# Kernel tuning notes

Hardware: AMD Instinct MI355X
Metric: run time of the kernel (lower is better)

The kernel has to match this reference:

```python
import jax, jax.numpy as jnp
import numpy as np

NUM_HEADS = 8
EPS = 1e-12  # torch F.normalize eps


def _l2norm(t):
    n = jnp.linalg.norm(t, axis=-1, keepdims=True)
    return t / jnp.maximum(n, EPS)


def setup_inputs() -> dict:
    key = jax.random.key(0)
    k1, k2, k3 = jax.random.split(key, 3)
    B, T, N, D = 16, 12, 1024, 128
    x = jax.random.normal(k1, (B, T, N, D), dtype=jnp.float32)
    # Linear(model_dim, 3*model_dim, bias=False): stored as (D, 3D) for x @ W
    W_qkv = jax.random.normal(k2, (D, 3 * D), dtype=jnp.float32) * (1.0 / np.sqrt(D))
    W_out = jax.random.normal(k3, (D, D), dtype=jnp.float32) * (1.0 / np.sqrt(D))
    b_out = jnp.zeros((D,), dtype=jnp.float32)
    return {"x": x, "W_qkv": W_qkv, "W_out": W_out, "b_out": b_out}


def reference(x, W_qkv, W_out, b_out):
    B, T, N, D = x.shape
    H = NUM_HEADS
    hd = D // H
    qkv = x @ W_qkv                                  # (B,T,N,3D)
    q, k, v = jnp.split(qkv, 3, axis=-1)
    # split heads + flatten (B,T) -> b = B*T, matching torch stack/flatten
    qs = _l2norm(q.reshape(B * T, N, H, hd))          # (b,N,H,m)
    ks = _l2norm(k.reshape(B * T, N, H, hd))
    vs = v.reshape(B * T, N, H, hd)
    # linear attention: running kv sum + normalizer
    kvs = jnp.einsum('blhm,blhd->bhmd', ks, vs)       # (b,H,m,d)
    attn_num = jnp.einsum('bnhm,bhmd->bnhd', qs, kvs) + N * vs
    ks_sum = jnp.sum(ks, axis=1)                      # (b,H,m)
    normalizer = jnp.einsum('bnhm,bhm->bnh', qs, ks_sum)[..., None] + N
    out = attn_num / normalizer                       # (b,N,H,d)
    out = out.reshape(B, T, N, D)
    return out @ W_out + b_out
```

## Files before the change

kernel.cpp:

```cpp
#include <hip/hip_runtime.h>
#include <hip/hip_bf16.h>

#define NBATCH 192
#define SEQ    1024
#define DIM    128
#define NH     8
#define EPS    1e-12f

typedef short bf16x8 __attribute__((ext_vector_type(8)));
typedef float f32x4  __attribute__((ext_vector_type(4)));

#define KVS_F   393216
#define ZERO_F  417792
#define WSWT_OFF ((size_t)ZERO_F * 4)
#define XB_OFF   (WSWT_OFF + 131072)
#define XB_SHPB  32768
#define WS_NEED  (XB_OFF + (size_t)768 * XB_SHPB * 2)

static __device__ __forceinline__ unsigned short f2bf(float f) {
    unsigned u = __builtin_bit_cast(unsigned, f);
    u += 0x7fff + ((u >> 16) & 1);
    return (unsigned short)(u >> 16);
}

static __device__ __forceinline__ unsigned pk2(float a, float b) {
    __hip_bfloat162 h = __float22bfloat162_rn(make_float2(a, b));
    unsigned r;
    __builtin_memcpy(&r, &h, 4);
    return r;
}
static __device__ __forceinline__ unsigned short bf1(float a) {
    __hip_bfloat16 h = __float2bfloat16(a);
    unsigned short r;
    __builtin_memcpy(&r, &h, 2);
    return r;
}

template <int CTRL>
static __device__ __forceinline__ float dpp_add(float v) {
    int j = __builtin_amdgcn_mov_dpp(__builtin_bit_cast(int, v), CTRL, 0xf, 0xf, false);
    return v + __builtin_bit_cast(float, j);
}
static __device__ __forceinline__ float r16sum(float v) {
    v = dpp_add<0xB1>(v);
    v = dpp_add<0x4E>(v);
    v = dpp_add<0x141>(v);
    v = dpp_add<0x140>(v);
    return v;
}

static __device__ __forceinline__ int strip_addr(int row, int el) {
    return row * 32 + ((((el >> 3) ^ (row & 3)) << 3) | (el & 7));
}

static __device__ __forceinline__ uint2 pack4(float a, float b, float c, float d) {
    uint2 r;
    r.x = pk2(a, b);
    r.y = pk2(c, d);
    return r;
}

static __device__ __forceinline__ bf16x8 cvt8(float4 a, float4 b) {
    uint4 u;
    u.x = pk2(a.x, a.y); u.y = pk2(a.z, a.w);
    u.z = pk2(b.x, b.y); u.w = pk2(b.z, b.w);
    return __builtin_bit_cast(bf16x8, u);
}

static __device__ __forceinline__ bf16x8 gfrag(const unsigned short* __restrict__ wT,
                                               int ct, int ks, int lane) {
    return *reinterpret_cast<const bf16x8*>(wT + ((ct * 4 + ks) * 64 + lane) * 8);
}

__global__ __launch_bounds__(256) void k0_prep(const float* __restrict__ Wqkv,
                                               const float* __restrict__ Wout,
                                               float* __restrict__ zero_p,
                                               unsigned short* __restrict__ wsWT) {
    int bid = blockIdx.x, t = threadIdx.x;
    if (bid < 1632) { zero_p[bid * 256 + t] = 0.0f; return; }
    int i = (bid - 1632) * 256 + t;
    int which = i >> 14, e = i & 16383;
    int j = e & 7, f = e >> 3;
    int n15 = f & 15, q = (f >> 4) & 3, ks = (f >> 6) & 3, ct = f >> 8;
    int k = ks * 32 + q * 8 + j, n = ct * 16 + n15;
    float v = (which < 3) ? Wqkv[k * 384 + which * 128 + n] : Wout[k * 128 + n];
    wsWT[i] = f2bf(v);
}

__global__ __launch_bounds__(512, 4) void k1_kv(const float* __restrict__ x,
                                                const unsigned short* __restrict__ wsWT,
                                                float* __restrict__ kvs_ws,
                                                float* __restrict__ kssum_ws,
                                                unsigned short* __restrict__ xb,
                                                int writeXb) {
    __shared__ float redf[16384];
    __shared__ unsigned short strips[8192];
    int t = threadIdx.x, w = t >> 6, lane = t & 63, q = lane >> 4, n15 = lane & 15;
    int b = blockIdx.x >> 2, seg = blockIdx.x & 3;
    const unsigned short* wkT = wsWT + 16384;
    const unsigned short* wvT = wsWT + 32768;
    unsigned short* knS = strips + w * 1024;
    unsigned short* vS  = knS + 512;

    bf16x8 ah[2][4];
#pragma unroll
    for (int rs = 0; rs < 2; ++rs) {
        int row = seg * 256 + w * 32 + rs * 16 + n15;
        const float* xr = x + (size_t)(b * SEQ + row) * DIM;
#pragma unroll
        for (int ks = 0; ks < 4; ++ks) {
            float4 p0 = *reinterpret_cast<const float4*>(xr + ks * 32 + q * 8);
            float4 p1 = *reinterpret_cast<const float4*>(xr + ks * 32 + q * 8 + 4);
            ah[rs][ks] = cvt8(p0, p1);
        }
    }
    if (writeXb) {
        unsigned short* xo = xb + (size_t)blockIdx.x * XB_SHPB + t * 8;
#pragma unroll
        for (int rs = 0; rs < 2; ++rs)
#pragma unroll
            for (int ks = 0; ks < 4; ++ks)
                *reinterpret_cast<uint4*>(xo + (rs * 4 + ks) * 4096) =
                    __builtin_bit_cast(uint4, ah[rs][ks]);
    }

#pragma unroll 1
    for (int ct = 0; ct < 8; ++ct) {
        f32x4 ka[2] = {(f32x4){0,0,0,0}, (f32x4){0,0,0,0}};
        f32x4 va[2] = {(f32x4){0,0,0,0}, (f32x4){0,0,0,0}};
#pragma unroll
        for (int ks = 0; ks < 4; ++ks) {
            bf16x8 kb = gfrag(wkT, ct, ks, lane);
            bf16x8 vb = gfrag(wvT, ct, ks, lane);
#pragma unroll
            for (int rs = 0; rs < 2; ++rs) {
                ka[rs] = __builtin_amdgcn_mfma_f32_16x16x32_bf16(ah[rs][ks], kb, ka[rs], 0, 0, 0);
                va[rs] = __builtin_amdgcn_mfma_f32_16x16x32_bf16(ah[rs][ks], vb, va[rs], 0, 0, 0);
            }
        }
        float ksum = 0.f;
#pragma unroll
        for (int rs = 0; rs < 2; ++rs) {
            float kn[4];
#pragma unroll
            for (int r = 0; r < 4; ++r) {
                float val = ka[rs][r];
                float ssq = r16sum(val * val);
                float di  = 1.0f / fmaxf(sqrtf(ssq), EPS);
                kn[r] = val * di;
                ksum += kn[r];
            }
            *reinterpret_cast<uint2*>(knS + strip_addr(n15, rs * 16 + q * 4)) =
                pack4(kn[0], kn[1], kn[2], kn[3]);
            *reinterpret_cast<uint2*>(vS + strip_addr(n15, rs * 16 + q * 4)) =
                pack4(va[rs][0], va[rs][1], va[rs][2], va[rs][3]);
        }
        bf16x8 aK = *reinterpret_cast<const bf16x8*>(knS + strip_addr(n15, q * 8));
        bf16x8 bV = *reinterpret_cast<const bf16x8*>(vS + strip_addr(n15, q * 8));
        f32x4 kacc = __builtin_amdgcn_mfma_f32_16x16x32_bf16(aK, bV, (f32x4){0,0,0,0}, 0, 0, 0);
#pragma unroll
        for (int r = 0; r < 4; ++r)
            redf[w * 2048 + ct * 256 + (q * 4 + r) * 16 + n15] = kacc[r];
        float s = ksum;
        s += __shfl_xor(s, 16); s += __shfl_xor(s, 32);
        if (lane < 16) atomicAdd(&kssum_ws[b * 128 + ct * 16 + n15], s);
    }

    __syncthreads();
#pragma unroll
    for (int i = 0; i < 4; ++i) {
        int el = i * 512 + t;
        float s = 0.f;
#pragma unroll
        for (int ww = 0; ww < 8; ++ww) s += redf[ww * 2048 + el];
        atomicAdd(&kvs_ws[b * 2048 + el], s);
    }
}

template <int XB>
__global__ __launch_bounds__(512, 4) void k2_out(const float* __restrict__ x,
                                                 const unsigned short* __restrict__ wsWT,
                                                 const float* __restrict__ kvs_ws,
                                                 const float* __restrict__ kssum_ws,
                                                 const float* __restrict__ bout,
                                                 float* __restrict__ out,
                                                 const unsigned short* __restrict__ xb) {
    __shared__ unsigned short lds[24576];
    unsigned short* kvsT   = lds;
    unsigned short* strips = lds + 4096;
    unsigned short* tile   = lds + 8192;
    int t = threadIdx.x, w = t >> 6, lane = t & 63, q = lane >> 4, n15 = lane & 15;
    int b = blockIdx.x >> 2, seg = blockIdx.x & 3, rowbase = seg * 256;
    const unsigned short* wqT = wsWT;
    const unsigned short* wvT = wsWT + 32768;
    const unsigned short* woT = wsWT + 49152;

    {
        int row = t >> 2, part = t & 3, h = row >> 4, d = row & 15;
        unsigned es[8];
#pragma unroll
        for (int j = 0; j < 8; j += 2) {
            int m0 = part * 8 + j;
            float lo = (m0     < 16) ? kvs_ws[b * 2048 + h * 256 + m0 * 16 + d]       : 0.f;
            float hi = (m0 + 1 < 16) ? kvs_ws[b * 2048 + h * 256 + (m0 + 1) * 16 + d] : 0.f;
            es[j] = pk2(lo, hi);
        }
        uint4 v = {es[0], es[2], es[4], es[6]};
        *reinterpret_cast<uint4*>(kvsT + row * 32 + ((part ^ (row & 3)) << 3)) = v;
    }

    bf16x8 ah[2][4];
    if (XB) {
        const unsigned short* xi = xb + (size_t)blockIdx.x * XB_SHPB + t * 8;
#pragma unroll
        for (int rs = 0; rs < 2; ++rs)
#pragma unroll
            for (int ks = 0; ks < 4; ++ks)
                ah[rs][ks] = *reinterpret_cast<const bf16x8*>(xi + (rs * 4 + ks) * 4096);
    } else {
#pragma unroll
        for (int rs = 0; rs < 2; ++rs) {
            int row = rowbase + w * 32 + rs * 16 + n15;
            const float* xr = x + (size_t)(b * SEQ + row) * DIM;
#pragma unroll
            for (int ks = 0; ks < 4; ++ks) {
                float4 p0 = *reinterpret_cast<const float4*>(xr + ks * 32 + q * 8);
                float4 p1 = *reinterpret_cast<const float4*>(xr + ks * 32 + q * 8 + 4);
                ah[rs][ks] = cvt8(p0, p1);
            }
        }
    }

    unsigned short* myS = strips + w * 512;
    unsigned short* tw  = tile + w * 2048;
    {
        uint2 z = {0, 0};
        *reinterpret_cast<uint2*>(myS + strip_addr(n15, 16 + q * 4)) = z;
    }
    __syncthreads();

#pragma unroll
    for (int rs = 0; rs < 2; ++rs) {
#pragma unroll 1
        for (int h = 0; h < 8; ++h) {
            float kssh = kssum_ws[b * 128 + h * 16 + n15];
            f32x4 qa = (f32x4){0,0,0,0};
            f32x4 va = (f32x4){0,0,0,0};
#pragma unroll
            for (int ks = 0; ks < 4; ++ks) {
                bf16x8 qb = gfrag(wqT, h, ks, lane);
                bf16x8 vb = gfrag(wvT, h, ks, lane);
                qa = __builtin_amdgcn_mfma_f32_16x16x32_bf16(ah[rs][ks], qb, qa, 0, 0, 0);
                va = __builtin_amdgcn_mfma_f32_16x16x32_bf16(ah[rs][ks], vb, va, 0, 0, 0);
            }
            float pv[4];
#pragma unroll
            for (int r = 0; r < 4; ++r) {
                float val = qa[r];
                float ssq = r16sum(val * val);
                float tt  = r16sum(val * kssh);
                float di  = 1.0f / fmaxf(sqrtf(ssq), EPS);
                float inv = 1.0f / (tt * di + (float)SEQ);
                pv[r] = val * di * inv;
                va[r] *= (float)SEQ * inv;
            }
#pragma unroll
            for (int r = 0; r < 4; ++r)
                myS[strip_addr(q * 4 + r, n15)] = bf1(pv[r]);
            bf16x8 aq = *reinterpret_cast<const bf16x8*>(myS + strip_addr(n15, q * 8));
            bf16x8 bk = *reinterpret_cast<const bf16x8*>(kvsT + strip_addr(h * 16 + n15, q * 8));
            va = __builtin_amdgcn_mfma_f32_16x16x32_bf16(aq, bk, va, 0, 0, 0);
#pragma unroll
            for (int r = 0; r < 4; ++r) {
                int rt = q * 4 + r;
                int colg = h * 2 + (n15 >> 3);
                tw[rt * 128 + (((colg ^ rt) << 3) | (n15 & 7))] = bf1(va[r]);
            }
        }

        bf16x8 ap[4];
#pragma unroll
        for (int ks = 0; ks < 4; ++ks)
            ap[ks] = *reinterpret_cast<const bf16x8*>(
                tw + n15 * 128 + ((((ks << 2) + q) ^ n15) << 3));
#pragma unroll 1
        for (int ct = 0; ct < 8; ++ct) {
            f32x4 oa = (f32x4){0,0,0,0};
#pragma unroll
            for (int ks = 0; ks < 4; ++ks) {
                bf16x8 bb = gfrag(woT, ct, ks, lane);
                oa = __builtin_amdgcn_mfma_f32_16x16x32_bf16(ap[ks], bb, oa, 0, 0, 0);
            }
            float bo = bout[ct * 16 + n15];
#pragma unroll
            for (int r = 0; r < 4; ++r) {
                int row = rowbase + w * 32 + rs * 16 + q * 4 + r;
                out[(size_t)(b * SEQ + row) * DIM + ct * 16 + n15] = oa[r] + bo;
            }
        }
    }
}

extern "C" void kernel_launch(void* const* d_in, const int* in_sizes, int n_in,
                              void* d_out, int out_size, void* d_ws, size_t ws_size,
                              hipStream_t stream) {
    const float* x    = (const float*)d_in[0];
    const float* Wqkv = (const float*)d_in[1];
    const float* Wout = (const float*)d_in[2];
    const float* bout = (const float*)d_in[3];
    float* out = (float*)d_out;

    float* kvs_ws   = (float*)d_ws;
    float* kssum_ws = kvs_ws + KVS_F;
    unsigned short* wsWT = (unsigned short*)((char*)d_ws + WSWT_OFF);
    unsigned short* xb   = (unsigned short*)((char*)d_ws + XB_OFF);
    int use_xb = (ws_size >= WS_NEED) ? 1 : 0;

    k0_prep<<<dim3(1888), dim3(256), 0, stream>>>(Wqkv, Wout, kvs_ws, wsWT);
    k1_kv<<<dim3(768), dim3(512), 0, stream>>>(x, wsWT, kvs_ws, kssum_ws, xb, use_xb);
    if (use_xb)
        k2_out<1><<<dim3(768), dim3(512), 0, stream>>>(x, wsWT, kvs_ws, kssum_ws, bout, out, xb);
    else
        k2_out<0><<<dim3(768), dim3(512), 0, stream>>>(x, wsWT, kvs_ws, kssum_ws, bout, out, xb);
}
```

Baseline: 284.7 us.

## Replace kvs atomics with per-block partials, drop bf16 x cache, prefetch weights

k1 now writes its per-segment kv partial sums to separate workspace slots instead of doing atomicAdd into a shared buffer. k2 sums the four segment partials when loading kvs, which also removes the large zeroing pass from the prep kernel. The bf16 copy of x that k1 wrote and k2 read is dropped, so k2 re-reads fp32 x one row strip at a time, lowering register pressure. The h loop now prefetches the next head's Wq fragments and ks_sum, trading less atomic and zeroing traffic for extra fp32 reads of x.

```diff
diff --git a/kernel.cpp b/kernel.cpp
--- a/kernel.cpp
+++ b/kernel.cpp
@@ -10,12 +10,9 @@
 typedef short bf16x8 __attribute__((ext_vector_type(8)));
 typedef float f32x4  __attribute__((ext_vector_type(4)));
 
-#define KVS_F   393216
-#define ZERO_F  417792
-#define WSWT_OFF ((size_t)ZERO_F * 4)
-#define XB_OFF   (WSWT_OFF + 131072)
-#define XB_SHPB  32768
-#define WS_NEED  (XB_OFF + (size_t)768 * XB_SHPB * 2)
+#define KVSP_F   1572864
+#define KSSUM_F  24576
+#define WSWT_OFF ((size_t)(KVSP_F + KSSUM_F) * 4)
 
 static __device__ __forceinline__ unsigned short f2bf(float f) {
     unsigned u = __builtin_bit_cast(unsigned, f);
@@ -74,11 +71,10 @@
 
 __global__ __launch_bounds__(256) void k0_prep(const float* __restrict__ Wqkv,
                                                const float* __restrict__ Wout,
-                                               float* __restrict__ zero_p,
+                                               float* __restrict__ kssum_ws,
                                                unsigned short* __restrict__ wsWT) {
-    int bid = blockIdx.x, t = threadIdx.x;
-    if (bid < 1632) { zero_p[bid * 256 + t] = 0.0f; return; }
-    int i = (bid - 1632) * 256 + t;
+    int i = blockIdx.x * 256 + threadIdx.x;
+    if (i < KSSUM_F) kssum_ws[i] = 0.0f;
     int which = i >> 14, e = i & 16383;
     int j = e & 7, f = e >> 3;
     int n15 = f & 15, q = (f >> 4) & 3, ks = (f >> 6) & 3, ct = f >> 8;
@@ -89,10 +85,8 @@
 
 __global__ __launch_bounds__(512, 4) void k1_kv(const float* __restrict__ x,
                                                 const unsigned short* __restrict__ wsWT,
-                                                float* __restrict__ kvs_ws,
-                                                float* __restrict__ kssum_ws,
-                                                unsigned short* __restrict__ xb,
-                                                int writeXb) {
+                                                float* __restrict__ kvs_part,
+                                                float* __restrict__ kssum_ws) {
     __shared__ float redf[16384];
     __shared__ unsigned short strips[8192];
     int t = threadIdx.x, w = t >> 6, lane = t & 63, q = lane >> 4, n15 = lane & 15;
@@ -114,15 +108,6 @@
             ah[rs][ks] = cvt8(p0, p1);
         }
     }
-    if (writeXb) {
-        unsigned short* xo = xb + (size_t)blockIdx.x * XB_SHPB + t * 8;
-#pragma unroll
-        for (int rs = 0; rs < 2; ++rs)
-#pragma unroll
-            for (int ks = 0; ks < 4; ++ks)
-                *reinterpret_cast<uint4*>(xo + (rs * 4 + ks) * 4096) =
-                    __builtin_bit_cast(uint4, ah[rs][ks]);
-    }
 
 #pragma unroll 1
     for (int ct = 0; ct < 8; ++ct) {
@@ -167,24 +152,23 @@
     }
 
     __syncthreads();
+    float* myPart = kvs_part + (size_t)blockIdx.x * 2048;
 #pragma unroll
     for (int i = 0; i < 4; ++i) {
         int el = i * 512 + t;
         float s = 0.f;
 #pragma unroll
         for (int ww = 0; ww < 8; ++ww) s += redf[ww * 2048 + el];
-        atomicAdd(&kvs_ws[b * 2048 + el], s);
-    }
-}
-
-template <int XB>
+        myPart[el] = s;
+    }
+}
+
 __global__ __launch_bounds__(512, 4) void k2_out(const float* __restrict__ x,
                                                  const unsigned short* __restrict__ wsWT,
-                                                 const float* __restrict__ kvs_ws,
+                                                 const float* __restrict__ kvs_part,
                                                  const float* __restrict__ kssum_ws,
                                                  const float* __restrict__ bout,
-                                                 float* __restrict__ out,
-                                                 const unsigned short* __restrict__ xb) {
+                                                 float* __restrict__ out) {
     __shared__ unsigned short lds[24576];
     unsigned short* kvsT   = lds;
     unsigned short* strips = lds + 4096;
@@ -197,38 +181,21 @@
 
     {
         int row = t >> 2, part = t & 3, h = row >> 4, d = row & 15;
+        const float* kp = kvs_part + (size_t)b * 4 * 2048;
         unsigned es[8];
 #pragma unroll
         for (int j = 0; j < 8; j += 2) {
             int m0 = part * 8 + j;
-            float lo = (m0     < 16) ? kvs_ws[b * 2048 + h * 256 + m0 * 16 + d]       : 0.f;
-            float hi = (m0 + 1 < 16) ? kvs_ws[b * 2048 + h * 256 + (m0 + 1) * 16 + d] : 0.f;
+            float lo = 0.f, hi = 0.f;
+#pragma unroll
+            for (int s = 0; s < 4; ++s) {
+                if (m0     < 16) lo += kp[s * 2048 + h * 256 + m0 * 16 + d];
+                if (m0 + 1 < 16) hi += kp[s * 2048 + h * 256 + (m0 + 1) * 16 + d];
+            }
             es[j] = pk2(lo, hi);
         }
         uint4 v = {es[0], es[2], es[4], es[6]};
         *reinterpret_cast<uint4*>(kvsT + row * 32 + ((part ^ (row & 3)) << 3)) = v;
-    }
-
-    bf16x8 ah[2][4];
-    if (XB) {
-        const unsigned short* xi = xb + (size_t)blockIdx.x * XB_SHPB + t * 8;
-#pragma unroll
-        for (int rs = 0; rs < 2; ++rs)
-#pragma unroll
-            for (int ks = 0; ks < 4; ++ks)
-                ah[rs][ks] = *reinterpret_cast<const bf16x8*>(xi + (rs * 4 + ks) * 4096);
-    } else {
-#pragma unroll
-        for (int rs = 0; rs < 2; ++rs) {
-            int row = rowbase + w * 32 + rs * 16 + n15;
-            const float* xr = x + (size_t)(b * SEQ + row) * DIM;
-#pragma unroll
-            for (int ks = 0; ks < 4; ++ks) {
-                float4 p0 = *reinterpret_cast<const float4*>(xr + ks * 32 + q * 8);
-                float4 p1 = *reinterpret_cast<const float4*>(xr + ks * 32 + q * 8 + 4);
-                ah[rs][ks] = cvt8(p0, p1);
-            }
-        }
     }
 
     unsigned short* myS = strips + w * 512;
@@ -239,20 +206,49 @@
     }
     __syncthreads();
 
-#pragma unroll
+    bf16x8 qb[4];
+#pragma unroll
+    for (int ks = 0; ks < 4; ++ks) qb[ks] = gfrag(wqT, 0, ks, lane);
+    float kssh = kssum_ws[b * 128 + n15];
+
+#pragma unroll 1
     for (int rs = 0; rs < 2; ++rs) {
+        bf16x8 ahc[4];
+        {
+            int row = rowbase + w * 32 + rs * 16 + n15;
+            const float* xr = x + (size_t)(b * SEQ + row) * DIM;
+#pragma unroll
+            for (int ks = 0; ks < 4; ++ks) {
+                float4 p0 = *reinterpret_cast<const float4*>(xr + ks * 32 + q * 8);
+                float4 p1 = *reinterpret_cast<const float4*>(xr + ks * 32 + q * 8 + 4);
+                ahc[ks] = cvt8(p0, p1);
+            }
+        }
+
 #pragma unroll 1
         for (int h = 0; h < 8; ++h) {
-            float kssh = kssum_ws[b * 128 + h * 16 + n15];
+            bf16x8 vb0 = gfrag(wvT, h, 0, lane);
+            bf16x8 vb1 = gfrag(wvT, h, 1, lane);
+            bf16x8 vb2 = gfrag(wvT, h, 2, lane);
+            bf16x8 vb3 = gfrag(wvT, h, 3, lane);
             f32x4 qa = (f32x4){0,0,0,0};
+            qa = __builtin_amdgcn_mfma_f32_16x16x32_bf16(ahc[0], qb[0], qa, 0, 0, 0);
+            qa = __builtin_amdgcn_mfma_f32_16x16x32_bf16(ahc[1], qb[1], qa, 0, 0, 0);
+            qa = __builtin_amdgcn_mfma_f32_16x16x32_bf16(ahc[2], qb[2], qa, 0, 0, 0);
+            qa = __builtin_amdgcn_mfma_f32_16x16x32_bf16(ahc[3], qb[3], qa, 0, 0, 0);
             f32x4 va = (f32x4){0,0,0,0};
-#pragma unroll
-            for (int ks = 0; ks < 4; ++ks) {
-                bf16x8 qb = gfrag(wqT, h, ks, lane);
-                bf16x8 vb = gfrag(wvT, h, ks, lane);
-                qa = __builtin_amdgcn_mfma_f32_16x16x32_bf16(ah[rs][ks], qb, qa, 0, 0, 0);
-                va = __builtin_amdgcn_mfma_f32_16x16x32_bf16(ah[rs][ks], vb, va, 0, 0, 0);
-            }
+            va = __builtin_amdgcn_mfma_f32_16x16x32_bf16(ahc[0], vb0, va, 0, 0, 0);
+            va = __builtin_amdgcn_mfma_f32_16x16x32_bf16(ahc[1], vb1, va, 0, 0, 0);
+            va = __builtin_amdgcn_mfma_f32_16x16x32_bf16(ahc[2], vb2, va, 0, 0, 0);
+            va = __builtin_amdgcn_mfma_f32_16x16x32_bf16(ahc[3], vb3, va, 0, 0, 0);
+
+            int hn = (h + 1) & 7;
+            bf16x8 nqb0 = gfrag(wqT, hn, 0, lane);
+            bf16x8 nqb1 = gfrag(wqT, hn, 1, lane);
+            bf16x8 nqb2 = gfrag(wqT, hn, 2, lane);
+            bf16x8 nqb3 = gfrag(wqT, hn, 3, lane);
+            float nkss = kssum_ws[b * 128 + hn * 16 + n15];
+
             float pv[4];
 #pragma unroll
             for (int r = 0; r < 4; ++r) {
@@ -276,6 +272,8 @@
                 int colg = h * 2 + (n15 >> 3);
                 tw[rt * 128 + (((colg ^ rt) << 3) | (n15 & 7))] = bf1(va[r]);
             }
+            qb[0] = nqb0; qb[1] = nqb1; qb[2] = nqb2; qb[3] = nqb3;
+            kssh = nkss;
         }
 
         bf16x8 ap[4];
@@ -310,16 +308,11 @@
     const float* bout = (const float*)d_in[3];
     float* out = (float*)d_out;
 
-    float* kvs_ws   = (float*)d_ws;
-    float* kssum_ws = kvs_ws + KVS_F;
+    float* kvs_part = (float*)d_ws;
+    float* kssum_ws = kvs_part + KVSP_F;
     unsigned short* wsWT = (unsigned short*)((char*)d_ws + WSWT_OFF);
-    unsigned short* xb   = (unsigned short*)((char*)d_ws + XB_OFF);
-    int use_xb = (ws_size >= WS_NEED) ? 1 : 0;
-
-    k0_prep<<<dim3(1888), dim3(256), 0, stream>>>(Wqkv, Wout, kvs_ws, wsWT);
-    k1_kv<<<dim3(768), dim3(512), 0, stream>>>(x, wsWT, kvs_ws, kssum_ws, xb, use_xb);
-    if (use_xb)
-        k2_out<1><<<dim3(768), dim3(512), 0, stream>>>(x, wsWT, kvs_ws, kssum_ws, bout, out, xb);
-    else
-        k2_out<0><<<dim3(768), dim3(512), 0, stream>>>(x, wsWT, kvs_ws, kssum_ws, bout, out, xb);
-}
+
+    k0_prep<<<dim3(256), dim3(256), 0, stream>>>(Wqkv, Wout, kssum_ws, wsWT);
+    k1_kv<<<dim3(768), dim3(512), 0, stream>>>(x, wsWT, kvs_part, kssum_ws);
+    k2_out<<<dim3(768), dim3(512), 0, stream>>>(x, wsWT, kvs_part, kssum_ws, bout, out);
+}
```

After: 281.5 us. Within noise of the previous version (-1.1%).
